# Kernel optimization log

Hardware: AMD Instinct MI355X
Metric: run time of the kernel (lower is better)

## Reference

```python
import jax, jax.numpy as jnp
import numpy as np

NUM_USER = 200000
NUM_ITEM = 200000
DIM_E = 64
DIM_FEAT = 128
B = 16384
NUM_NEG = 16
TEMP = 0.2
LR_LAMBDA = 0.5
NUM_SAMPLE = 0.5


def _l2norm(x, eps=1e-12):
    # F.normalize(x, dim=1): x / max(||x||_2, eps)
    n = jnp.sqrt(jnp.sum(x * x, axis=1, keepdims=True))
    return x / jnp.maximum(n, eps)


def setup_inputs() -> dict:
    key = jax.random.key(0)
    ks = jax.random.split(key, 9)
    G = 1 + NUM_NEG
    N = B * G
    v_feat = jax.random.normal(ks[0], (NUM_ITEM, DIM_FEAT), dtype=jnp.float32)
    id_embedding = jax.random.normal(ks[1], (NUM_USER + NUM_ITEM, DIM_E), dtype=jnp.float32) * 0.05
    W1 = jax.random.normal(ks[2], (DIM_FEAT, 256), dtype=jnp.float32) * (1.0 / np.sqrt(DIM_FEAT))
    b1 = jnp.zeros((256,), dtype=jnp.float32)
    W2 = jax.random.normal(ks[3], (256, DIM_E), dtype=jnp.float32) * (1.0 / np.sqrt(256.0))
    b2 = jnp.zeros((DIM_E,), dtype=jnp.float32)
    user_tensor = jax.random.randint(ks[4], (B, G), 0, NUM_USER, dtype=jnp.int32)
    # item ids are global ids in [num_user, num_user + num_item)
    item_tensor = jax.random.randint(ks[5], (B, G), NUM_USER, NUM_USER + NUM_ITEM, dtype=jnp.int32)
    num_to_replace = int(N * NUM_SAMPLE)
    rand_index = jax.random.randint(ks[6], (num_to_replace,), 0, N, dtype=jnp.int32)
    return {
        'v_feat': v_feat, 'id_embedding': id_embedding,
        'W1': W1, 'b1': b1, 'W2': W2, 'b2': b2,
        'user_tensor': user_tensor, 'item_tensor': item_tensor,
        'rand_index': rand_index,
    }


def _encoder(v_feat, W1, b1, W2, b2):
    vf = _l2norm(v_feat)                      # F.normalize in __init__
    h = jax.nn.leaky_relu(vf @ W1 + b1)       # negative_slope=0.01 (torch default)
    return h @ W2 + b2                        # [num_item, dim_E]


def _loss_contrastive(anchor, allv):
    # exp(<a, v>/T) reshaped to [B, 1+num_neg]; col 0 is positive
    s = jnp.exp(jnp.sum(anchor * allv, axis=1) / TEMP).reshape(-1, 1 + NUM_NEG)
    pos = s[:, 0]
    tot = jnp.sum(s, axis=1)
    return jnp.mean(-jnp.log(pos / (tot + 1e-8) + 1e-8))


def reference(v_feat, id_embedding, W1, b1, W2, b2, user_tensor, item_tensor, rand_index):
    G = 1 + NUM_NEG
    feature = _encoder(v_feat, W1, b1, W2, b2)           # [num_item, dim_E]
    pos_item = jnp.repeat(item_tensor[:, :1], G, axis=1).reshape(-1)  # [B*G]
    uflat = user_tensor.reshape(-1)
    iflat = item_tensor.reshape(-1)
    item_idx = jnp.clip(iflat - NUM_USER, 0, feature.shape[0] - 1)
    all_item_feat = feature[item_idx]                    # [B*G, dim_E]
    user_emb = id_embedding[uflat]
    pos_emb = id_embedding[pos_item]
    all_emb = id_embedding[iflat]
    head_feat = _l2norm(all_item_feat)
    head_embed = _l2norm(pos_emb)
    # replace a random subset of embedding rows with encoded features
    all_item_input = all_emb.at[rand_index].set(all_item_feat[rand_index])
    l1 = _loss_contrastive(head_embed, head_feat)
    l2 = _loss_contrastive(user_emb, all_item_input)
    return LR_LAMBDA * l1 + (1.0 - LR_LAMBDA) * l2
```

## Files before the change

### kernel.cpp

```cpp
#include <hip/hip_runtime.h>
#include <hip/hip_bf16.h>

typedef __bf16 bf16_t;
typedef __bf16 bf16x8 __attribute__((ext_vector_type(8)));
typedef __bf16 bf16x4 __attribute__((ext_vector_type(4)));
typedef float f32x4 __attribute__((ext_vector_type(4)));
typedef unsigned int u32;

#define NUM_USER 200000
#define NUM_ITEM 200000
#define DIM_E 64
#define DIM_FEAT 128
#define HID 256
#define BATCH 16384
#define GG 17
#define NN (BATCH * GG)
#define NREP 139264
#define W1LP 136
#define W2LP 264
#define NWAVES 2048
#define NSP 6250

__global__ __launch_bounds__(256) void prep3_kernel(
    const float* __restrict__ W1, const float* __restrict__ W2,
    const int* __restrict__ rand_index,
    bf16_t* __restrict__ W1t, bf16_t* __restrict__ W2t,
    unsigned char* __restrict__ mask)
{
    const int t = blockIdx.x * 256 + threadIdx.x;
    if (t < HID * DIM_FEAT) {
        const int n = t >> 7, k = t & 127;
        W1t[t] = (bf16_t)W1[k * HID + n];
    }
    if (t < DIM_E * HID) {
        const int n = t >> 8, c = t & 255;
        const int b = c >> 5, p = c & 31;
        const int Q = p >> 3, j = p & 7;
        const int k = b * 32 + Q * 4 + (j & 3) + ((j >> 2) << 4);
        W2t[t] = (bf16_t)W2[k * DIM_E + n];
    }
    if (t < NREP) mask[rand_index[t]] = 1;
}

__global__ __launch_bounds__(512, 2) void encoder10_kernel(
    const float* __restrict__ vfeat,
    const bf16_t* __restrict__ W1t, const float* __restrict__ b1v,
    const bf16_t* __restrict__ W2t, const float* __restrict__ b2v,
    bf16_t* __restrict__ featB)
{
    const int tid  = threadIdx.x;
    const int wave = tid >> 6;
    const int lane = tid & 63;
    const int r    = lane & 15;
    const int Q    = lane >> 4;

    __shared__ bf16_t w1s[256 * W1LP];
    __shared__ bf16_t w2s[64 * W2LP];
    __shared__ float  b1s[HID];
    __shared__ float  b2s[DIM_E];

    for (int c = tid; c < 4096; c += 512) {
        const int n = c >> 4, ks = c & 15;
        *reinterpret_cast<uint4*>(&w1s[n * W1LP + ks * 8]) =
            reinterpret_cast<const uint4*>(W1t)[c];
    }
    for (int c = tid; c < 2048; c += 512) {
        const int n = c >> 5, ks = c & 31;
        *reinterpret_cast<uint4*>(&w2s[n * W2LP + ks * 8]) =
            reinterpret_cast<const uint4*>(W2t)[c];
    }
    if (tid < HID) b1s[tid] = b1v[tid];
    if (tid < DIM_E) b2s[tid] = b2v[tid];
    __syncthreads();

    int sp = blockIdx.x * 8 + wave;

    float4 v0[2][4], v1[2][4];
    {
        const size_t row0 = (size_t)sp * 32;
#pragma unroll
        for (int s = 0; s < 2; ++s) {
            const float* rp = vfeat + (row0 + s * 16 + r) * DIM_FEAT + Q * 8;
#pragma unroll
            for (int ks = 0; ks < 4; ++ks) {
                v0[s][ks] = *reinterpret_cast<const float4*>(rp + ks * 32);
                v1[s][ks] = *reinterpret_cast<const float4*>(rp + ks * 32 + 4);
            }
        }
    }

    while (sp < NSP) {
        const size_t row0 = (size_t)sp * 32;

        bf16x8 af[2][4];
#pragma unroll
        for (int s = 0; s < 2; ++s) {
            float ss = 0.f;
#pragma unroll
            for (int ks = 0; ks < 4; ++ks) {
                ss += v0[s][ks].x * v0[s][ks].x + v0[s][ks].y * v0[s][ks].y
                    + v0[s][ks].z * v0[s][ks].z + v0[s][ks].w * v0[s][ks].w;
                ss += v1[s][ks].x * v1[s][ks].x + v1[s][ks].y * v1[s][ks].y
                    + v1[s][ks].z * v1[s][ks].z + v1[s][ks].w * v1[s][ks].w;
            }
            ss += __shfl_xor(ss, 16, 64);
            ss += __shfl_xor(ss, 32, 64);
            const float inv = 1.0f / fmaxf(sqrtf(ss), 1e-12f);
#pragma unroll
            for (int ks = 0; ks < 4; ++ks) {
                bf16x8 v;
                v[0] = (bf16_t)(v0[s][ks].x * inv); v[1] = (bf16_t)(v0[s][ks].y * inv);
                v[2] = (bf16_t)(v0[s][ks].z * inv); v[3] = (bf16_t)(v0[s][ks].w * inv);
                v[4] = (bf16_t)(v1[s][ks].x * inv); v[5] = (bf16_t)(v1[s][ks].y * inv);
                v[6] = (bf16_t)(v1[s][ks].z * inv); v[7] = (bf16_t)(v1[s][ks].w * inv);
                af[s][ks] = v;
            }
        }

        const int spn = sp + NWAVES;
        if (spn < NSP) {
            const size_t nr0 = (size_t)spn * 32;
#pragma unroll
            for (int s = 0; s < 2; ++s) {
                const float* rp = vfeat + (nr0 + s * 16 + r) * DIM_FEAT + Q * 8;
#pragma unroll
                for (int ks = 0; ks < 4; ++ks) {
                    v0[s][ks] = *reinterpret_cast<const float4*>(rp + ks * 32);
                    v1[s][ks] = *reinterpret_cast<const float4*>(rp + ks * 32 + 4);
                }
            }
        }

        f32x4 acc2[2][4];
#pragma unroll
        for (int s = 0; s < 2; ++s)
#pragma unroll
            for (int n2 = 0; n2 < 4; ++n2) acc2[s][n2] = (f32x4){0.f, 0.f, 0.f, 0.f};

#pragma unroll 2
        for (int t = 0; t < 8; ++t) {
            u32 pk[2][2][2];
#pragma unroll
            for (int h = 0; h < 2; ++h) {
                const int nt = t * 2 + h;
                const bf16_t* bp = &w1s[(nt * 16 + r) * W1LP + Q * 8];
                bf16x8 w1f[4];
#pragma unroll
                for (int ks = 0; ks < 4; ++ks)
                    w1f[ks] = *reinterpret_cast<const bf16x8*>(bp + ks * 32);
                const float4 bias1 = *reinterpret_cast<const float4*>(&b1s[nt * 16 + Q * 4]);
#pragma unroll
                for (int s = 0; s < 2; ++s) {
                    f32x4 a1 = (f32x4){0.f, 0.f, 0.f, 0.f};
#pragma unroll
                    for (int ks = 0; ks < 4; ++ks)
                        a1 = __builtin_amdgcn_mfma_f32_16x16x32_bf16(w1f[ks], af[s][ks], a1, 0, 0, 0);
                    bf16x4 hv4;
#pragma unroll
                    for (int i = 0; i < 4; ++i) {
                        float hv = a1[i] + ((const float*)&bias1)[i];
                        hv = hv >= 0.f ? hv : 0.01f * hv;
                        hv4[i] = (bf16_t)hv;
                    }
                    const uint2 u = __builtin_bit_cast(uint2, hv4);
                    pk[s][h][0] = u.x;
                    pk[s][h][1] = u.y;
                }
            }
            bf16x8 w2f[4];
#pragma unroll
            for (int n2 = 0; n2 < 4; ++n2)
                w2f[n2] = *reinterpret_cast<const bf16x8*>(
                    &w2s[(n2 * 16 + r) * W2LP + t * 32 + Q * 8]);
#pragma unroll
            for (int s = 0; s < 2; ++s) {
                uint4 bu;
                bu.x = pk[s][0][0];
                bu.y = pk[s][0][1];
                bu.z = pk[s][1][0];
                bu.w = pk[s][1][1];
                const bf16x8 hfrag = __builtin_bit_cast(bf16x8, bu);
#pragma unroll
                for (int n2 = 0; n2 < 4; ++n2)
                    acc2[s][n2] = __builtin_amdgcn_mfma_f32_16x16x32_bf16(w2f[n2], hfrag, acc2[s][n2], 0, 0, 0);
            }
        }

#pragma unroll
        for (int n2 = 0; n2 < 4; ++n2) {
            const float4 bias2 = *reinterpret_cast<const float4*>(&b2s[n2 * 16 + Q * 4]);
#pragma unroll
            for (int s = 0; s < 2; ++s) {
                bf16x4 o;
                o[0] = (bf16_t)(acc2[s][n2][0] + bias2.x);
                o[1] = (bf16_t)(acc2[s][n2][1] + bias2.y);
                o[2] = (bf16_t)(acc2[s][n2][2] + bias2.z);
                o[3] = (bf16_t)(acc2[s][n2][3] + bias2.w);
                *reinterpret_cast<bf16x4*>(
                    featB + (row0 + s * 16 + r) * DIM_E + n2 * 16 + Q * 4) = o;
            }
        }
        sp = spn;
    }
}

__global__ __launch_bounds__(256) void loss_elem4_kernel(
    const bf16_t* __restrict__ featB, const float* __restrict__ id_emb,
    const int* __restrict__ user_t, const int* __restrict__ item_t,
    const unsigned char* __restrict__ mask,
    float* __restrict__ s1, float* __restrict__ s2)
{
    const int kq = threadIdx.x & 3;
    const int c  = blockIdx.x * 64 + (threadIdx.x >> 2);

#pragma unroll
    for (int half = 0; half < 2; ++half) {
        const int nn = c + half * (NN / 2);
        const int b  = nn / GG;
        const int u  = user_t[nn];
        const int it = item_t[nn];
        const int pos = item_t[b * GG];
        int fidx = min(max(it - NUM_USER, 0), NUM_ITEM - 1);
        const bool rep = mask[nn] != 0;

        const bf16x8* fp = reinterpret_cast<const bf16x8*>(featB + (size_t)fidx * DIM_E + kq * 16);
        const float4* pp = reinterpret_cast<const float4*>(id_emb + (size_t)pos * DIM_E) + kq * 4;
        const float4* up = reinterpret_cast<const float4*>(id_emb + (size_t)u   * DIM_E) + kq * 4;
        const float4* ip = reinterpret_cast<const float4*>(id_emb + (size_t)it  * DIM_E) + kq * 4;

        const bf16x8 f8a = fp[0];
        const bf16x8 f8b = fp[1];

        float x = 0.f, y = 0.f, z = 0.f, w = 0.f;
#pragma unroll
        for (int j = 0; j < 4; ++j) {
            const float4 p  = pp[j];
            const float4 uu = up[j];
            const float4 iv = ip[j];
            const bf16x8 fb = (j < 2) ? f8a : f8b;
            float f0 = (float)fb[(j & 1) * 4 + 0];
            float f1 = (float)fb[(j & 1) * 4 + 1];
            float f2 = (float)fb[(j & 1) * 4 + 2];
            float f3 = (float)fb[(j & 1) * 4 + 3];
            const float a0 = rep ? f0 : iv.x;
            const float a1 = rep ? f1 : iv.y;
            const float a2 = rep ? f2 : iv.z;
            const float a3 = rep ? f3 : iv.w;
            x += f0 * f0 + f1 * f1 + f2 * f2 + f3 * f3;
            y += p.x * p.x + p.y * p.y + p.z * p.z + p.w * p.w;
            z += p.x * f0 + p.y * f1 + p.z * f2 + p.w * f3;
            w += uu.x * a0 + uu.y * a1 + uu.z * a2 + uu.w * a3;
        }
#pragma unroll
        for (int off = 1; off <= 2; off <<= 1) {
            x += __shfl_xor(x, off, 64);
            y += __shfl_xor(y, off, 64);
            z += __shfl_xor(z, off, 64);
            w += __shfl_xor(w, off, 64);
        }
        if (kq == 0) {
            const float dot1 = z / (fmaxf(sqrtf(x), 1e-12f) * fmaxf(sqrtf(y), 1e-12f));
            s1[nn] = __expf(dot1 * 5.0f);
            s2[nn] = __expf(w * 5.0f);
        }
    }
}

__global__ __launch_bounds__(256) void loss_reduce_kernel(
    const float* __restrict__ s1, const float* __restrict__ s2,
    float* __restrict__ out)
{
    const int b = blockIdx.x * 256 + threadIdx.x;
    float tot1 = 0.f, tot2 = 0.f, p1 = 0.f, p2 = 0.f;
#pragma unroll
    for (int g = 0; g < GG; ++g) {
        const float a1 = s1[b * GG + g];
        const float a2 = s2[b * GG + g];
        if (g == 0) { p1 = a1; p2 = a2; }
        tot1 += a1; tot2 += a2;
    }
    const float l1 = -logf(p1 / (tot1 + 1e-8f) + 1e-8f);
    const float l2 = -logf(p2 / (tot2 + 1e-8f) + 1e-8f);
    float v = 0.5f * l1 + 0.5f * l2;
#pragma unroll
    for (int off = 32; off > 0; off >>= 1) v += __shfl_xor(v, off, 64);
    __shared__ float red[4];
    const int wave = threadIdx.x >> 6, lane = threadIdx.x & 63;
    if (lane == 0) red[wave] = v;
    __syncthreads();
    if (threadIdx.x == 0)
        atomicAdd(out, (red[0] + red[1] + red[2] + red[3]) * (1.0f / BATCH));
}

extern "C" void kernel_launch(void* const* d_in, const int* in_sizes, int n_in,
                              void* d_out, int out_size, void* d_ws, size_t ws_size,
                              hipStream_t stream)
{
    (void)in_sizes; (void)n_in; (void)out_size; (void)ws_size;
    const float* v_feat    = (const float*)d_in[0];
    const float* id_emb    = (const float*)d_in[1];
    const float* W1        = (const float*)d_in[2];
    const float* b1        = (const float*)d_in[3];
    const float* W2        = (const float*)d_in[4];
    const float* b2        = (const float*)d_in[5];
    const int*   user_t    = (const int*)d_in[6];
    const int*   item_t    = (const int*)d_in[7];
    const int*   rand_idx  = (const int*)d_in[8];

    char* ws = (char*)d_ws;
    bf16_t*        W1t      = (bf16_t*)(ws + 0);
    bf16_t*        W2t      = (bf16_t*)(ws + 65536);
    unsigned char* mask     = (unsigned char*)(ws + 98304);
    float*         s1       = (float*)(ws + 376832);
    float*         s2       = (float*)(ws + 1490944);
    bf16_t*        featB    = (bf16_t*)(ws + 2605056);

    hipMemsetAsync(mask, 0, NN, stream);
    hipMemsetAsync(d_out, 0, sizeof(float), stream);
    prep3_kernel<<<544, 256, 0, stream>>>(W1, W2, rand_idx, W1t, W2t, mask);
    encoder10_kernel<<<256, 512, 0, stream>>>(v_feat, W1t, b1, W2t, b2, featB);
    loss_elem4_kernel<<<2176, 256, 0, stream>>>(featB, id_emb, user_t, item_t, mask, s1, s2);
    loss_reduce_kernel<<<64, 256, 0, stream>>>(s1, s2, (float*)d_out);
}
```

Before: 277.2 us.

## Fuse per-element loss and per-row reduction into one kernel

Merges the elementwise similarity kernel and the row-reduction kernel into one. Each group of 8 threads owns one batch row, loads the positive embedding and its norm once, and splits the 17 candidates across two thread pairs. This removes the s1/s2 intermediate buffers, one kernel launch, and the redundant per-element reload of the positive embedding. In exchange there are fewer blocks (512 instead of 2176), so less parallelism is available to hide memory latency on the gathers.

```diff
diff --git a/kernel.cpp b/kernel.cpp
--- a/kernel.cpp
+++ b/kernel.cpp
@@ -204,89 +204,88 @@
     }
 }
 
-__global__ __launch_bounds__(256) void loss_elem4_kernel(
+__global__ __launch_bounds__(256) void loss_fused_kernel(
     const bf16_t* __restrict__ featB, const float* __restrict__ id_emb,
     const int* __restrict__ user_t, const int* __restrict__ item_t,
     const unsigned char* __restrict__ mask,
-    float* __restrict__ s1, float* __restrict__ s2)
+    float* __restrict__ out)
 {
-    const int kq = threadIdx.x & 3;
-    const int c  = blockIdx.x * 64 + (threadIdx.x >> 2);
-
-#pragma unroll
-    for (int half = 0; half < 2; ++half) {
-        const int nn = c + half * (NN / 2);
-        const int b  = nn / GG;
+    const int lane = threadIdx.x & 63;
+    const int kq   = lane & 3;
+    const int par  = (lane >> 2) & 1;
+    const int b    = blockIdx.x * 32 + (threadIdx.x >> 3);
+
+    const int pos = item_t[b * GG];
+    const float4* pp = reinterpret_cast<const float4*>(id_emb + (size_t)pos * DIM_E) + kq * 4;
+    const float4 pr0 = pp[0], pr1 = pp[1], pr2 = pp[2], pr3 = pp[3];
+    float y = pr0.x*pr0.x + pr0.y*pr0.y + pr0.z*pr0.z + pr0.w*pr0.w
+            + pr1.x*pr1.x + pr1.y*pr1.y + pr1.z*pr1.z + pr1.w*pr1.w
+            + pr2.x*pr2.x + pr2.y*pr2.y + pr2.z*pr2.z + pr2.w*pr2.w
+            + pr3.x*pr3.x + pr3.y*pr3.y + pr3.z*pr3.z + pr3.w*pr3.w;
+    y += __shfl_xor(y, 1, 64);
+    y += __shfl_xor(y, 2, 64);
+    const float ny = fmaxf(sqrtf(y), 1e-12f);
+
+    float tot1 = 0.f, tot2 = 0.f, ps1 = 0.f, ps2 = 0.f;
+    for (int g = par; g < GG; g += 2) {
+        const int nn = b * GG + g;
         const int u  = user_t[nn];
         const int it = item_t[nn];
-        const int pos = item_t[b * GG];
-        int fidx = min(max(it - NUM_USER, 0), NUM_ITEM - 1);
         const bool rep = mask[nn] != 0;
-
-        const bf16x8* fp = reinterpret_cast<const bf16x8*>(featB + (size_t)fidx * DIM_E + kq * 16);
-        const float4* pp = reinterpret_cast<const float4*>(id_emb + (size_t)pos * DIM_E) + kq * 4;
-        const float4* up = reinterpret_cast<const float4*>(id_emb + (size_t)u   * DIM_E) + kq * 4;
-        const float4* ip = reinterpret_cast<const float4*>(id_emb + (size_t)it  * DIM_E) + kq * 4;
-
+        const int fidx = min(max(it - NUM_USER, 0), NUM_ITEM - 1);
+
+        const bf16x8* fp = reinterpret_cast<const bf16x8*>(
+            featB + (size_t)fidx * DIM_E + kq * 16);
+        const float4* up = reinterpret_cast<const float4*>(id_emb + (size_t)u  * DIM_E) + kq * 4;
+        const float4* ip = reinterpret_cast<const float4*>(id_emb + (size_t)it * DIM_E) + kq * 4;
         const bf16x8 f8a = fp[0];
         const bf16x8 f8b = fp[1];
 
-        float x = 0.f, y = 0.f, z = 0.f, w = 0.f;
+        float x = 0.f, z = 0.f, w = 0.f;
 #pragma unroll
         for (int j = 0; j < 4; ++j) {
-            const float4 p  = pp[j];
+            const float4 pv = (j == 0) ? pr0 : (j == 1) ? pr1 : (j == 2) ? pr2 : pr3;
             const float4 uu = up[j];
             const float4 iv = ip[j];
             const bf16x8 fb = (j < 2) ? f8a : f8b;
-            float f0 = (float)fb[(j & 1) * 4 + 0];
-            float f1 = (float)fb[(j & 1) * 4 + 1];
-            float f2 = (float)fb[(j & 1) * 4 + 2];
-            float f3 = (float)fb[(j & 1) * 4 + 3];
+            const float f0 = (float)fb[(j & 1) * 4 + 0];
+            const float f1 = (float)fb[(j & 1) * 4 + 1];
+            const float f2 = (float)fb[(j & 1) * 4 + 2];
+            const float f3 = (float)fb[(j & 1) * 4 + 3];
             const float a0 = rep ? f0 : iv.x;
             const float a1 = rep ? f1 : iv.y;
             const float a2 = rep ? f2 : iv.z;
             const float a3 = rep ? f3 : iv.w;
             x += f0 * f0 + f1 * f1 + f2 * f2 + f3 * f3;
-            y += p.x * p.x + p.y * p.y + p.z * p.z + p.w * p.w;
-            z += p.x * f0 + p.y * f1 + p.z * f2 + p.w * f3;
+            z += pv.x * f0 + pv.y * f1 + pv.z * f2 + pv.w * f3;
             w += uu.x * a0 + uu.y * a1 + uu.z * a2 + uu.w * a3;
         }
-#pragma unroll
-        for (int off = 1; off <= 2; off <<= 1) {
-            x += __shfl_xor(x, off, 64);
-            y += __shfl_xor(y, off, 64);
-            z += __shfl_xor(z, off, 64);
-            w += __shfl_xor(w, off, 64);
-        }
-        if (kq == 0) {
-            const float dot1 = z / (fmaxf(sqrtf(x), 1e-12f) * fmaxf(sqrtf(y), 1e-12f));
-            s1[nn] = __expf(dot1 * 5.0f);
-            s2[nn] = __expf(w * 5.0f);
-        }
-    }
-}
-
-__global__ __launch_bounds__(256) void loss_reduce_kernel(
-    const float* __restrict__ s1, const float* __restrict__ s2,
-    float* __restrict__ out)
-{
-    const int b = blockIdx.x * 256 + threadIdx.x;
-    float tot1 = 0.f, tot2 = 0.f, p1 = 0.f, p2 = 0.f;
-#pragma unroll
-    for (int g = 0; g < GG; ++g) {
-        const float a1 = s1[b * GG + g];
-        const float a2 = s2[b * GG + g];
-        if (g == 0) { p1 = a1; p2 = a2; }
-        tot1 += a1; tot2 += a2;
-    }
-    const float l1 = -logf(p1 / (tot1 + 1e-8f) + 1e-8f);
-    const float l2 = -logf(p2 / (tot2 + 1e-8f) + 1e-8f);
-    float v = 0.5f * l1 + 0.5f * l2;
-#pragma unroll
-    for (int off = 32; off > 0; off >>= 1) v += __shfl_xor(v, off, 64);
+        x += __shfl_xor(x, 1, 64); x += __shfl_xor(x, 2, 64);
+        z += __shfl_xor(z, 1, 64); z += __shfl_xor(z, 2, 64);
+        w += __shfl_xor(w, 1, 64); w += __shfl_xor(w, 2, 64);
+
+        const float dot1 = z / (fmaxf(sqrtf(x), 1e-12f) * ny);
+        const float e1 = __expf(dot1 * 5.0f);
+        const float e2 = __expf(w * 5.0f);
+        if (g == 0) { ps1 = e1; ps2 = e2; }
+        tot1 += e1; tot2 += e2;
+    }
+    tot1 += __shfl_xor(tot1, 4, 64);
+    tot2 += __shfl_xor(tot2, 4, 64);
+
+    float v = 0.f;
+    if ((lane & 7) == 0) {
+        const float l1 = -logf(ps1 / (tot1 + 1e-8f) + 1e-8f);
+        const float l2 = -logf(ps2 / (tot2 + 1e-8f) + 1e-8f);
+        v = 0.5f * l1 + 0.5f * l2;
+    }
+    v += __shfl_xor(v, 8, 64);
+    v += __shfl_xor(v, 16, 64);
+    v += __shfl_xor(v, 32, 64);
+
     __shared__ float red[4];
-    const int wave = threadIdx.x >> 6, lane = threadIdx.x & 63;
-    if (lane == 0) red[wave] = v;
+    const int wv = threadIdx.x >> 6;
+    if (lane == 0) red[wv] = v;
     __syncthreads();
     if (threadIdx.x == 0)
         atomicAdd(out, (red[0] + red[1] + red[2] + red[3]) * (1.0f / BATCH));
@@ -311,14 +310,11 @@
     bf16_t*        W1t      = (bf16_t*)(ws + 0);
     bf16_t*        W2t      = (bf16_t*)(ws + 65536);
     unsigned char* mask     = (unsigned char*)(ws + 98304);
-    float*         s1       = (float*)(ws + 376832);
-    float*         s2       = (float*)(ws + 1490944);
     bf16_t*        featB    = (bf16_t*)(ws + 2605056);
 
     hipMemsetAsync(mask, 0, NN, stream);
     hipMemsetAsync(d_out, 0, sizeof(float), stream);
     prep3_kernel<<<544, 256, 0, stream>>>(W1, W2, rand_idx, W1t, W2t, mask);
     encoder10_kernel<<<256, 512, 0, stream>>>(v_feat, W1t, b1, W2t, b2, featB);
-    loss_elem4_kernel<<<2176, 256, 0, stream>>>(featB, id_emb, user_t, item_t, mask, s1, s2);
-    loss_reduce_kernel<<<64, 256, 0, stream>>>(s1, s2, (float*)d_out);
+    loss_fused_kernel<<<512, 256, 0, stream>>>(featB, id_emb, user_t, item_t, mask, (float*)d_out);
 }
```

New measurement: 268.8 us. 3.0% less time.
